# Optimization experiments

Hardware: AMD Instinct MI355X
Metric: run time of the kernel (lower is better)

The kernel has to match this reference:

```python
import jax, jax.numpy as jnp
import numpy as np

B, N = 32768, 512

def setup_inputs() -> dict:
    key = jax.random.key(0)
    k1, k2, k3, k4 = jax.random.split(key, 4)
    log_sigma_hat = jax.random.normal(k1, (B, N), dtype=jnp.float32)
    sigma = jax.random.normal(k2, (B, N), dtype=jnp.float32)
    SR = jax.random.normal(k3, (N,), dtype=jnp.float32)
    # well-conditioned invertible Gamma (covariance-like): A A^T / N + I
    A = jax.random.normal(k4, (N, N), dtype=jnp.float32)
    Gamma = A @ A.T / N + jnp.eye(N, dtype=jnp.float32)
    return {"log_sigma_hat": log_sigma_hat, "sigma": sigma, "SR": SR, "Gamma": Gamma, "k": 12}

def reference(log_sigma_hat, sigma, SR, Gamma, k):
    # r[t] = exp(sigma[t]) / exp(log_sigma_hat[t])  -> [B, N]
    r = jnp.exp(sigma - log_sigma_hat)
    Gamma_inv = jnp.linalg.inv(Gamma)
    v = Gamma_inv @ SR           # [N]  Gamma^{-1} SR
    u = Gamma_inv.T @ SR         # [N]  (SR^T Gamma^{-1})^T
    # first  = SR^T Gamma^{-1} diag(r) SR / k = sum(u * r * SR)
    first = (r * (u * SR)).sum(axis=-1) / k
    # second = SR^T Gamma^{-1} diag(r) Gamma diag(r) Gamma^{-1} SR / (2k)
    w = r * v                                     # [B, N] = diag(r) v
    Gw = jnp.einsum('ij,bj->bi', Gamma, w)        # [B, N] = Gamma diag(r) v
    second = (u * (r * Gw)).sum(axis=-1) / (2 * k)
    utils = first - second                        # [B]
    return -utils.mean()
```

## Files before the change

### kernel.cpp

```cpp
#include <hip/hip_runtime.h>
#include <hip/hip_bf16.h>
#include <stdint.h>

#define BB 32768
#define NN 512
#define CHEB_IT 10
#define NSB 16
#define NTILE 10
#define NPART 64

typedef __attribute__((ext_vector_type(8))) short bf16x8;
typedef __attribute__((ext_vector_type(4))) float f32x4;

__device__ __forceinline__ void gld_lds16(const void* g, void* l) {
  typedef __attribute__((address_space(1))) const unsigned int gas_u32;
  typedef __attribute__((address_space(3))) unsigned int las_u32;
  __builtin_amdgcn_global_load_lds((gas_u32*)(uintptr_t)g,
                                   (las_u32*)(uint32_t)(uintptr_t)l, 16, 0, 0);
}

__device__ __forceinline__ unsigned short f2bf(float x) {
  __hip_bfloat16 h = __float2bfloat16(x);
  return *reinterpret_cast<unsigned short*>(&h);
}

__device__ __forceinline__ float bf2f(unsigned short u) {
  return __uint_as_float(((unsigned)u) << 16);
}

__device__ __forceinline__ float wave_reduce(float v) {
#pragma unroll
  for (int off = 32; off > 0; off >>= 1) v += __shfl_xor(v, off, 64);
  return v;
}

__device__ void cheb_phase(const unsigned short* __restrict__ Gbf,
                           const float* __restrict__ SR, float* __restrict__ v_out,
                           float* __restrict__ pglob, unsigned int* __restrict__ ctr,
                           char* smraw) {
  unsigned short* Gs = (unsigned short*)smraw;
  float* sp = (float*)(smraw + 32768);
  float* red = sp + 512;
  const int t = threadIdx.x;
  const int m = blockIdx.x;
#pragma unroll
  for (int h = 0; h < 4; ++h) {
    const int row = h * 128 + (t >> 2), sc = t & 3;
    gld_lds16(Gbf + (size_t)row * NN + m * 32 + sc * 8, Gs + row * 32 + sc * 8);
  }
  const float theta = 3.16f, delta = 2.19f;
  const float sigma1 = theta / delta;
  float rho = delta / theta;
  float x = 0.f, r = 0.f, p = 0.f;
  if (t < 32) {
    float s = SR[m * 32 + t];
    r = s;
    p = s * (1.0f / theta);
  }
  sp[t] = SR[t] * (1.0f / theta);
  __syncthreads();
  for (int k = 0; k < CHEB_IT; ++k) {
    const int c2 = (t & 15) * 2, jseg = t >> 4;
    float a0 = 0.f, a1 = 0.f;
#pragma unroll
    for (int i = 0; i < 16; ++i) {
      const int j = jseg * 16 + i;
      const unsigned g2 = *(const unsigned*)(Gs + j * 32 + c2);
      const float pv = sp[j];
      a0 += bf2f((unsigned short)(g2 & 0xffffu)) * pv;
      a1 += bf2f((unsigned short)(g2 >> 16)) * pv;
    }
    a0 += __shfl_xor(a0, 16, 64); a0 += __shfl_xor(a0, 32, 64);
    a1 += __shfl_xor(a1, 16, 64); a1 += __shfl_xor(a1, 32, 64);
    const int lane = t & 63, wv = t >> 6;
    if (lane < 16) {
      red[wv * 32 + lane * 2] = a0;
      red[wv * 32 + lane * 2 + 1] = a1;
    }
    __syncthreads();
    const float rho_new = 1.f / (2.f * sigma1 - rho);
    if (t < 32) {
      float ap = 0.f;
#pragma unroll
      for (int w = 0; w < 8; ++w) ap += red[w * 32 + t];
      x += p;
      r -= ap;
      p = rho_new * rho * p + (2.f * rho_new / delta) * r;
      if (k < CHEB_IT - 1)
        __hip_atomic_store(pglob + (k & 1) * 512 + m * 32 + t, p,
                           __ATOMIC_RELAXED, __HIP_MEMORY_SCOPE_AGENT);
    }
    rho = rho_new;
    if (k == CHEB_IT - 1) break;
    __threadfence();
    __syncthreads();
    if (t == 0) {
      __hip_atomic_fetch_add(ctr, 1u, __ATOMIC_RELEASE, __HIP_MEMORY_SCOPE_AGENT);
      const unsigned tgt = (unsigned)NSB * (unsigned)(k + 1);
      int guard = 0;
      while (__hip_atomic_load(ctr, __ATOMIC_ACQUIRE, __HIP_MEMORY_SCOPE_AGENT) < tgt) {
        if (++guard > (1 << 27)) break;
        __builtin_amdgcn_s_sleep(8);
      }
    }
    __syncthreads();
    sp[t] = __hip_atomic_load(pglob + (k & 1) * 512 + t, __ATOMIC_RELAXED,
                              __HIP_MEMORY_SCOPE_AGENT);
    __syncthreads();
  }
  if (t < 32) v_out[m * 32 + t] = x;
}

__global__ __launch_bounds__(256) void k0_prep(
    const float* __restrict__ Gam, unsigned short* __restrict__ Gbf,
    float* __restrict__ small_zero) {
  const int t = threadIdx.x, b = blockIdx.x;
  const size_t base = ((size_t)b * 256 + t) * 8;
  float4 g0 = *(const float4*)(Gam + base);
  float4 g1 = *(const float4*)(Gam + base + 4);
  *(ushort4*)(Gbf + base) = make_ushort4(f2bf(g0.x), f2bf(g0.y), f2bf(g0.z), f2bf(g0.w));
  *(ushort4*)(Gbf + base + 4) = make_ushort4(f2bf(g1.x), f2bf(g1.y), f2bf(g1.z), f2bf(g1.w));
  if (b == 0)
    for (int i = t; i < 5888; i += 256) small_zero[i] = 0.f;
}

#define TSTRIDE 132
__global__ __launch_bounds__(512) void k1_rt(
    const float* __restrict__ lsh, const float* __restrict__ sig,
    unsigned short* __restrict__ Rt, float* __restrict__ colsum) {
  __shared__ __align__(16) float sm[4736];
  unsigned short* tile = (unsigned short*)sm;
  float* redc = sm + 4224;
  const int t = threadIdx.x;
  const int r = t >> 3, cg = t & 7;
  const int jr = t >> 3, cc = t & 7;
  const size_t bb = (size_t)blockIdx.x * 64;
  for (int jt = 0; jt < 4; ++jt) {
    const int j0 = jt * 128;
    const size_t off = (bb + r) * NN + j0 + cg * 16;
    float4 s0 = *(const float4*)(sig + off);
    float4 s1 = *(const float4*)(sig + off + 4);
    float4 s2 = *(const float4*)(sig + off + 8);
    float4 s3 = *(const float4*)(sig + off + 12);
    float4 l0 = *(const float4*)(lsh + off);
    float4 l1 = *(const float4*)(lsh + off + 4);
    float4 l2 = *(const float4*)(lsh + off + 8);
    float4 l3 = *(const float4*)(lsh + off + 12);
    ushort4 w0 = make_ushort4(f2bf(__expf(s0.x - l0.x)), f2bf(__expf(s0.y - l0.y)),
                              f2bf(__expf(s0.z - l0.z)), f2bf(__expf(s0.w - l0.w)));
    ushort4 w1 = make_ushort4(f2bf(__expf(s1.x - l1.x)), f2bf(__expf(s1.y - l1.y)),
                              f2bf(__expf(s1.z - l1.z)), f2bf(__expf(s1.w - l1.w)));
    ushort4 w2 = make_ushort4(f2bf(__expf(s2.x - l2.x)), f2bf(__expf(s2.y - l2.y)),
                              f2bf(__expf(s2.z - l2.z)), f2bf(__expf(s2.w - l2.w)));
    ushort4 w3 = make_ushort4(f2bf(__expf(s3.x - l3.x)), f2bf(__expf(s3.y - l3.y)),
                              f2bf(__expf(s3.z - l3.z)), f2bf(__expf(s3.w - l3.w)));
    if (jt) __syncthreads();
    *(ushort4*)(&tile[r * TSTRIDE + cg * 16 + 0]) = w0;
    *(ushort4*)(&tile[r * TSTRIDE + cg * 16 + 4]) = w1;
    *(ushort4*)(&tile[r * TSTRIDE + cg * 16 + 8]) = w2;
    *(ushort4*)(&tile[r * TSTRIDE + cg * 16 + 12]) = w3;
    __syncthreads();
#pragma unroll
    for (int pass = 0; pass < 2; ++pass) {
      const int j = jr + pass * 64;
      unsigned int u[4];
      float csum = 0.f;
#pragma unroll
      for (int q = 0; q < 4; ++q) {
        unsigned int lo = tile[(cc * 8 + 2 * q) * TSTRIDE + j];
        unsigned int hi = tile[(cc * 8 + 2 * q + 1) * TSTRIDE + j];
        u[q] = lo | (hi << 16);
        csum += bf2f((unsigned short)lo) + bf2f((unsigned short)hi);
      }
      *(uint4*)(Rt + (size_t)(j0 + j) * BB + bb + cc * 8) =
          make_uint4(u[0], u[1], u[2], u[3]);
      redc[t] = csum;
      __syncthreads();
      if (t < 64) {
        float s = 0.f;
#pragma unroll
        for (int q = 0; q < 8; ++q) s += redc[t * 8 + q];
        atomicAdd(&colsum[(blockIdx.x & 7) * NN + j0 + pass * 64 + t], s);
      }
      __syncthreads();
    }
  }
}

__global__ __launch_bounds__(512) void k2_syrk(
    const unsigned short* __restrict__ Rt, const unsigned short* __restrict__ Gbf,
    const float* __restrict__ SR, unsigned short* __restrict__ Cpart,
    float* __restrict__ v_out, float* __restrict__ pglob,
    unsigned int* __restrict__ ctr) {
  __shared__ __align__(16) char smraw[65536];
  if (blockIdx.x < NSB) {
    cheb_phase(Gbf, SR, v_out, pglob, ctr, smraw);
    return;
  }
  unsigned short* smem = (unsigned short*)smraw;
  const int wb = blockIdx.x - NSB;
  const int kc = wb / NTILE, tt = wb % NTILE;
  const int ti = (int)((0x3221110000ULL >> (4 * tt)) & 0xF);
  const int tj = (int)((0x3323213210ULL >> (4 * tt)) & 0xF);
  const int i0 = ti * 128, j0 = tj * 128;
  const int diag = (ti == tj);
  const size_t b0 = (size_t)kc * 512;
  const int t = threadIdx.x, lane = t & 63, wv = t >> 6;
  const int wi = (wv & 3) * 32, wj = (wv >> 2) * 64;
  const int lm = lane & 15, lq = lane >> 4;
  const int xr = lm & 7;
  const int srow = t >> 3, sc = t & 7;
  const int scol = (sc ^ (srow & 7)) * 8;
  f32x4 acc[2][4];
#pragma unroll
  for (int a = 0; a < 2; ++a)
#pragma unroll
    for (int b = 0; b < 4; ++b) acc[a][b] = (f32x4){0.f, 0.f, 0.f, 0.f};

#define STAGE(kk, buf)                                                              \
  {                                                                                 \
    unsigned short* As_ = smem + (buf)*16384;                                       \
    unsigned short* Bs_ = diag ? As_ : As_ + 8192;                                  \
    gld_lds16(Rt + (size_t)(i0 + srow) * BB + b0 + (kk) + scol,                     \
              As_ + srow * 64 + sc * 8);                                            \
    gld_lds16(Rt + (size_t)(i0 + 64 + srow) * BB + b0 + (kk) + scol,                \
              As_ + (64 + srow) * 64 + sc * 8);                                     \
    if (!diag) {                                                                    \
      gld_lds16(Rt + (size_t)(j0 + srow) * BB + b0 + (kk) + scol,                   \
                Bs_ + srow * 64 + sc * 8);                                          \
      gld_lds16(Rt + (size_t)(j0 + 64 + srow) * BB + b0 + (kk) + scol,              \
                Bs_ + (64 + srow) * 64 + sc * 8);                                   \
    }                                                                               \
  }

  STAGE(0, 0);
  __syncthreads();
  for (int c = 0; c < 8; ++c) {
    if (c < 7) STAGE((c + 1) * 64, (c + 1) & 1);
    const unsigned short* As = smem + (c & 1) * 16384;
    const unsigned short* Bs = diag ? As : As + 8192;
#pragma unroll
    for (int s = 0; s < 2; ++s) {
      bf16x8 af[2], bfr[4];
#pragma unroll
      for (int g = 0; g < 2; ++g)
        af[g] = *(const bf16x8*)(As + (wi + g * 16 + lm) * 64 + ((s * 4 + lq) ^ xr) * 8);
#pragma unroll
      for (int g = 0; g < 4; ++g)
        bfr[g] = *(const bf16x8*)(Bs + (wj + g * 16 + lm) * 64 + ((s * 4 + lq) ^ xr) * 8);
#pragma unroll
      for (int gm = 0; gm < 2; ++gm)
#pragma unroll
        for (int gn = 0; gn < 4; ++gn)
          acc[gm][gn] = __builtin_amdgcn_mfma_f32_16x16x32_bf16(af[gm], bfr[gn], acc[gm][gn], 0, 0, 0);
    }
    __syncthreads();
  }
#undef STAGE

  unsigned short* Cw = Cpart + (size_t)kc * NN * NN;
#pragma unroll
  for (int gm = 0; gm < 2; ++gm) {
    const int rbase = i0 + wi + gm * 16 + lq * 4;
#pragma unroll
    for (int gn = 0; gn < 4; ++gn) {
      const int col = j0 + wj + gn * 16 + lm;
      Cw[(size_t)(rbase + 0) * NN + col] = f2bf(acc[gm][gn][0]);
      Cw[(size_t)(rbase + 1) * NN + col] = f2bf(acc[gm][gn][1]);
      Cw[(size_t)(rbase + 2) * NN + col] = f2bf(acc[gm][gn][2]);
      Cw[(size_t)(rbase + 3) * NN + col] = f2bf(acc[gm][gn][3]);
    }
  }
}

__global__ __launch_bounds__(256) void k3_contract(
    const float* __restrict__ Gamma, const unsigned short* __restrict__ Cpart,
    const float* __restrict__ v, float* __restrict__ secondsum) {
  __shared__ float red[4];
  const int t = threadIdx.x;
  const int tidx = blockIdx.x >> 4;
  const int sub = ((blockIdx.x & 15) << 10) + t * 4;
  const int ti = (int)((0x3221110000ULL >> (4 * tidx)) & 0xF);
  const int tj = (int)((0x3323213210ULL >> (4 * tidx)) & 0xF);
  const float w = (ti == tj) ? 1.f : 2.f;
  const int i = ti * 128 + (sub >> 7);
  const int j = tj * 128 + (sub & 127);
  const size_t e = (size_t)i * NN + j;
  float cx = 0, cy = 0, cz = 0, cw = 0;
  for (int pp = 0; pp < NPART; ++pp) {
    ushort4 u = *(const ushort4*)(Cpart + (size_t)pp * NN * NN + e);
    cx += bf2f(u.x); cy += bf2f(u.y); cz += bf2f(u.z); cw += bf2f(u.w);
  }
  float4 g = *(const float4*)(Gamma + e);
  float4 vj = *(const float4*)(v + j);
  float vi = v[i];
  float p = w * vi * (g.x * cx * vj.x + g.y * cy * vj.y + g.z * cz * vj.z + g.w * cw * vj.w);
  p = wave_reduce(p);
  if ((t & 63) == 0) red[t >> 6] = p;
  __syncthreads();
  if (t == 0) atomicAdd(secondsum, red[0] + red[1] + red[2] + red[3]);
}

__global__ __launch_bounds__(512) void k4_final(
    const float* __restrict__ colsum, const float* __restrict__ v,
    const float* __restrict__ SR, const float* __restrict__ secondsum,
    const int* __restrict__ kp, float* __restrict__ out) {
  __shared__ float red[8];
  const int t = threadIdx.x;
  float cs = 0;
#pragma unroll
  for (int bk = 0; bk < 8; ++bk) cs += colsum[bk * NN + t];
  float f = (cs * (1.0f / BB)) * v[t] * SR[t];
  f = wave_reduce(f);
  if ((t & 63) == 0) red[t >> 6] = f;
  __syncthreads();
  if (t == 0) {
    float first = 0;
#pragma unroll
    for (int i = 0; i < 8; ++i) first += red[i];
    float kk = (float)kp[0];
    float sec = secondsum[0] / ((float)BB * 2.0f * kk);
    out[0] = -(first / kk - sec);
  }
}

extern "C" void kernel_launch(void* const* d_in, const int* in_sizes, int n_in,
                              void* d_out, int out_size, void* d_ws, size_t ws_size,
                              hipStream_t stream) {
  const float* lsh = (const float*)d_in[0];
  const float* sig = (const float*)d_in[1];
  const float* SR = (const float*)d_in[2];
  const float* Gam = (const float*)d_in[3];
  const int* kp = (const int*)d_in[4];
  char* ws = (char*)d_ws;
  unsigned short* Cpart = (unsigned short*)ws;
  const size_t coff = (size_t)NPART * NN * NN * sizeof(unsigned short);
  float* colsum = (float*)(ws + coff);
  float* secsum = colsum + 4096;
  float* v = secsum + 64;
  unsigned int* ctr = (unsigned int*)(v + 512);
  float* pglob = (float*)(ctr + 16);
  unsigned short* Gbf = (unsigned short*)(ws + coff + (32 << 10));
  unsigned short* Rt = (unsigned short*)(ws + coff + (32 << 10) + (512 << 10));

  k0_prep<<<128, 256, 0, stream>>>(Gam, Gbf, colsum);
  k1_rt<<<512, 512, 0, stream>>>(lsh, sig, Rt, colsum);
  k2_syrk<<<NSB + NPART * NTILE, 512, 0, stream>>>(Rt, Gbf, SR, Cpart, v, pglob, ctr);
  k3_contract<<<160, 256, 0, stream>>>(Gam, Cpart, v, secsum);
  k4_final<<<1, 512, 0, stream>>>(colsum, v, SR, secsum, kp, (float*)d_out);
}
```

Before: 232.9 us.

## Split Chebyshev solve across kernels, halve SYRK partials with 4-stage pipeline

```diff
diff --git a/kernel.cpp b/kernel.cpp
--- a/kernel.cpp
+++ b/kernel.cpp
@@ -7,7 +7,9 @@
 #define CHEB_IT 10
 #define NSB 16
 #define NTILE 10
-#define NPART 64
+#define NPART 32
+#define BKC 32
+#define NCH 32
 
 typedef __attribute__((ext_vector_type(8))) short bf16x8;
 typedef __attribute__((ext_vector_type(4))) float f32x4;
@@ -34,10 +36,11 @@
   return v;
 }
 
-__device__ void cheb_phase(const unsigned short* __restrict__ Gbf,
-                           const float* __restrict__ SR, float* __restrict__ v_out,
-                           float* __restrict__ pglob, unsigned int* __restrict__ ctr,
-                           char* smraw) {
+__device__ void cheb_run(const unsigned short* __restrict__ Gbf,
+                         const float* __restrict__ SR, float* __restrict__ st,
+                         float* __restrict__ v_out, float* __restrict__ pglob,
+                         unsigned int* __restrict__ ctr, char* smraw,
+                         int k0i, int k1i) {
   unsigned short* Gs = (unsigned short*)smraw;
   float* sp = (float*)(smraw + 32768);
   float* red = sp + 512;
@@ -51,15 +54,25 @@
   const float theta = 3.16f, delta = 2.19f;
   const float sigma1 = theta / delta;
   float rho = delta / theta;
+  for (int q = 0; q < k0i; ++q) rho = 1.f / (2.f * sigma1 - rho);
   float x = 0.f, r = 0.f, p = 0.f;
-  if (t < 32) {
-    float s = SR[m * 32 + t];
-    r = s;
-    p = s * (1.0f / theta);
-  }
-  sp[t] = SR[t] * (1.0f / theta);
+  if (k0i == 0) {
+    if (t < 32) {
+      float s = SR[m * 32 + t];
+      r = s;
+      p = s * (1.0f / theta);
+    }
+    sp[t] = SR[t] * (1.0f / theta);
+  } else {
+    if (t < 32) {
+      x = st[m * 32 + t];
+      r = st[512 + m * 32 + t];
+      p = st[1024 + m * 32 + t];
+    }
+    sp[t] = st[1024 + t];
+  }
   __syncthreads();
-  for (int k = 0; k < CHEB_IT; ++k) {
+  for (int k = k0i; k < k1i; ++k) {
     const int c2 = (t & 15) * 2, jseg = t >> 4;
     float a0 = 0.f, a1 = 0.f;
 #pragma unroll
@@ -86,17 +99,17 @@
       x += p;
       r -= ap;
       p = rho_new * rho * p + (2.f * rho_new / delta) * r;
-      if (k < CHEB_IT - 1)
+      if (k + 1 < k1i)
         __hip_atomic_store(pglob + (k & 1) * 512 + m * 32 + t, p,
                            __ATOMIC_RELAXED, __HIP_MEMORY_SCOPE_AGENT);
     }
     rho = rho_new;
-    if (k == CHEB_IT - 1) break;
+    if (k + 1 >= k1i) break;
     __threadfence();
     __syncthreads();
     if (t == 0) {
       __hip_atomic_fetch_add(ctr, 1u, __ATOMIC_RELEASE, __HIP_MEMORY_SCOPE_AGENT);
-      const unsigned tgt = (unsigned)NSB * (unsigned)(k + 1);
+      const unsigned tgt = (unsigned)NSB * (unsigned)(k - k0i + 1);
       int guard = 0;
       while (__hip_atomic_load(ctr, __ATOMIC_ACQUIRE, __HIP_MEMORY_SCOPE_AGENT) < tgt) {
         if (++guard > (1 << 27)) break;
@@ -108,7 +121,13 @@
                               __HIP_MEMORY_SCOPE_AGENT);
     __syncthreads();
   }
-  if (t < 32) v_out[m * 32 + t] = x;
+  if (k1i >= CHEB_IT) {
+    if (t < 32) v_out[m * 32 + t] = x;
+  } else if (t < 32) {
+    st[m * 32 + t] = x;
+    st[512 + m * 32 + t] = r;
+    st[1024 + m * 32 + t] = p;
+  }
 }
 
 __global__ __launch_bounds__(256) void k0_prep(
@@ -121,20 +140,27 @@
   *(ushort4*)(Gbf + base) = make_ushort4(f2bf(g0.x), f2bf(g0.y), f2bf(g0.z), f2bf(g0.w));
   *(ushort4*)(Gbf + base + 4) = make_ushort4(f2bf(g1.x), f2bf(g1.y), f2bf(g1.z), f2bf(g1.w));
   if (b == 0)
-    for (int i = t; i < 5888; i += 256) small_zero[i] = 0.f;
+    for (int i = t; i < 7424; i += 256) small_zero[i] = 0.f;
 }
 
 #define TSTRIDE 132
 __global__ __launch_bounds__(512) void k1_rt(
     const float* __restrict__ lsh, const float* __restrict__ sig,
-    unsigned short* __restrict__ Rt, float* __restrict__ colsum) {
-  __shared__ __align__(16) float sm[4736];
-  unsigned short* tile = (unsigned short*)sm;
-  float* redc = sm + 4224;
+    const float* __restrict__ SR, const unsigned short* __restrict__ Gbf,
+    unsigned short* __restrict__ Rt, float* __restrict__ colsum,
+    float* __restrict__ st, float* __restrict__ pglob,
+    unsigned int* __restrict__ ctr) {
+  __shared__ __align__(16) char smraw[36864];
+  if (blockIdx.x < NSB) {
+    cheb_run(Gbf, SR, st, nullptr, pglob, ctr, smraw, 0, 5);
+    return;
+  }
+  unsigned short* tile = (unsigned short*)smraw;
   const int t = threadIdx.x;
   const int r = t >> 3, cg = t & 7;
   const int jr = t >> 3, cc = t & 7;
-  const size_t bb = (size_t)blockIdx.x * 64;
+  const int wb = blockIdx.x - NSB;
+  const size_t bb = (size_t)wb * 64;
   for (int jt = 0; jt < 4; ++jt) {
     const int j0 = jt * 128;
     const size_t off = (bb + r) * NN + j0 + cg * 16;
@@ -174,89 +200,92 @@
       }
       *(uint4*)(Rt + (size_t)(j0 + j) * BB + bb + cc * 8) =
           make_uint4(u[0], u[1], u[2], u[3]);
-      redc[t] = csum;
-      __syncthreads();
-      if (t < 64) {
-        float s = 0.f;
-#pragma unroll
-        for (int q = 0; q < 8; ++q) s += redc[t * 8 + q];
-        atomicAdd(&colsum[(blockIdx.x & 7) * NN + j0 + pass * 64 + t], s);
-      }
-      __syncthreads();
+      csum += __shfl_xor(csum, 1, 64);
+      csum += __shfl_xor(csum, 2, 64);
+      csum += __shfl_xor(csum, 4, 64);
+      if (cc == 0) atomicAdd(&colsum[(wb & 7) * NN + j0 + j], csum);
     }
   }
 }
 
 __global__ __launch_bounds__(512) void k2_syrk(
     const unsigned short* __restrict__ Rt, const unsigned short* __restrict__ Gbf,
-    const float* __restrict__ SR, unsigned short* __restrict__ Cpart,
-    float* __restrict__ v_out, float* __restrict__ pglob,
+    unsigned short* __restrict__ Cpart, float* __restrict__ v_out,
+    float* __restrict__ st, float* __restrict__ pglob,
     unsigned int* __restrict__ ctr) {
   __shared__ __align__(16) char smraw[65536];
   if (blockIdx.x < NSB) {
-    cheb_phase(Gbf, SR, v_out, pglob, ctr, smraw);
+    cheb_run(Gbf, nullptr, st, v_out, pglob, ctr, smraw, 5, CHEB_IT);
     return;
   }
   unsigned short* smem = (unsigned short*)smraw;
   const int wb = blockIdx.x - NSB;
-  const int kc = wb / NTILE, tt = wb % NTILE;
+  const int kc = (wb & 7) * 4 + (wb >> 3) / NTILE;
+  const int tt = (wb >> 3) % NTILE;
   const int ti = (int)((0x3221110000ULL >> (4 * tt)) & 0xF);
   const int tj = (int)((0x3323213210ULL >> (4 * tt)) & 0xF);
   const int i0 = ti * 128, j0 = tj * 128;
   const int diag = (ti == tj);
-  const size_t b0 = (size_t)kc * 512;
+  const size_t b0 = (size_t)kc * 1024;
   const int t = threadIdx.x, lane = t & 63, wv = t >> 6;
   const int wi = (wv & 3) * 32, wj = (wv >> 2) * 64;
   const int lm = lane & 15, lq = lane >> 4;
-  const int xr = lm & 7;
-  const int srow = t >> 3, sc = t & 7;
-  const int scol = (sc ^ (srow & 7)) * 8;
+  const int srow4 = t >> 2, sc4 = t & 3;
+  const int scol4 = (sc4 ^ (srow4 & 3)) * 8;
   f32x4 acc[2][4];
 #pragma unroll
   for (int a = 0; a < 2; ++a)
 #pragma unroll
     for (int b = 0; b < 4; ++b) acc[a][b] = (f32x4){0.f, 0.f, 0.f, 0.f};
 
-#define STAGE(kk, buf)                                                              \
-  {                                                                                 \
-    unsigned short* As_ = smem + (buf)*16384;                                       \
-    unsigned short* Bs_ = diag ? As_ : As_ + 8192;                                  \
-    gld_lds16(Rt + (size_t)(i0 + srow) * BB + b0 + (kk) + scol,                     \
-              As_ + srow * 64 + sc * 8);                                            \
-    gld_lds16(Rt + (size_t)(i0 + 64 + srow) * BB + b0 + (kk) + scol,                \
-              As_ + (64 + srow) * 64 + sc * 8);                                     \
-    if (!diag) {                                                                    \
-      gld_lds16(Rt + (size_t)(j0 + srow) * BB + b0 + (kk) + scol,                   \
-                Bs_ + srow * 64 + sc * 8);                                          \
-      gld_lds16(Rt + (size_t)(j0 + 64 + srow) * BB + b0 + (kk) + scol,              \
-                Bs_ + (64 + srow) * 64 + sc * 8);                                   \
-    }                                                                               \
-  }
-
-  STAGE(0, 0);
-  __syncthreads();
-  for (int c = 0; c < 8; ++c) {
-    if (c < 7) STAGE((c + 1) * 64, (c + 1) & 1);
-    const unsigned short* As = smem + (c & 1) * 16384;
-    const unsigned short* Bs = diag ? As : As + 8192;
-#pragma unroll
-    for (int s = 0; s < 2; ++s) {
-      bf16x8 af[2], bfr[4];
-#pragma unroll
-      for (int g = 0; g < 2; ++g)
-        af[g] = *(const bf16x8*)(As + (wi + g * 16 + lm) * 64 + ((s * 4 + lq) ^ xr) * 8);
-#pragma unroll
-      for (int g = 0; g < 4; ++g)
-        bfr[g] = *(const bf16x8*)(Bs + (wj + g * 16 + lm) * 64 + ((s * 4 + lq) ^ xr) * 8);
-#pragma unroll
-      for (int gm = 0; gm < 2; ++gm)
-#pragma unroll
-        for (int gn = 0; gn < 4; ++gn)
-          acc[gm][gn] = __builtin_amdgcn_mfma_f32_16x16x32_bf16(af[gm], bfr[gn], acc[gm][gn], 0, 0, 0);
-    }
-    __syncthreads();
-  }
-#undef STAGE
+#define STAGE2(g)                                                               \
+  {                                                                             \
+    unsigned short* As_ = smem + ((g) & 3) * 8192;                              \
+    const size_t kb = b0 + (size_t)(g) * BKC;                                   \
+    gld_lds16(Rt + (size_t)(i0 + srow4) * BB + kb + scol4,                      \
+              As_ + srow4 * 32 + sc4 * 8);                                      \
+    if (!diag)                                                                  \
+      gld_lds16(Rt + (size_t)(j0 + srow4) * BB + kb + scol4,                    \
+                As_ + 4096 + srow4 * 32 + sc4 * 8);                             \
+  }
+
+  STAGE2(0); STAGE2(1); STAGE2(2);
+  for (int c = 0; c < NCH; ++c) {
+    const int pend = (NCH - 1 - c) < 2 ? (NCH - 1 - c) : 2;
+    if (diag) {
+      if (pend == 2) asm volatile("s_waitcnt vmcnt(2)" ::: "memory");
+      else if (pend == 1) asm volatile("s_waitcnt vmcnt(1)" ::: "memory");
+      else asm volatile("s_waitcnt vmcnt(0)" ::: "memory");
+    } else {
+      if (pend == 2) asm volatile("s_waitcnt vmcnt(4)" ::: "memory");
+      else if (pend == 1) asm volatile("s_waitcnt vmcnt(2)" ::: "memory");
+      else asm volatile("s_waitcnt vmcnt(0)" ::: "memory");
+    }
+    __builtin_amdgcn_sched_barrier(0);
+    __builtin_amdgcn_s_barrier();
+    if (c + 3 < NCH) STAGE2(c + 3);
+    const unsigned short* As = smem + (c & 3) * 8192;
+    const unsigned short* Bs = diag ? As : As + 4096;
+    bf16x8 af[2], bfr[4];
+#pragma unroll
+    for (int g = 0; g < 2; ++g) {
+      const int row = wi + g * 16 + lm;
+      af[g] = *(const bf16x8*)(As + row * 32 + (lq ^ (row & 3)) * 8);
+    }
+#pragma unroll
+    for (int g = 0; g < 4; ++g) {
+      const int row = wj + g * 16 + lm;
+      bfr[g] = *(const bf16x8*)(Bs + row * 32 + (lq ^ (row & 3)) * 8);
+    }
+#pragma unroll
+    for (int gm = 0; gm < 2; ++gm)
+#pragma unroll
+      for (int gn = 0; gn < 4; ++gn)
+        acc[gm][gn] = __builtin_amdgcn_mfma_f32_16x16x32_bf16(af[gm], bfr[gn], acc[gm][gn], 0, 0, 0);
+    __builtin_amdgcn_sched_barrier(0);
+    __builtin_amdgcn_s_barrier();
+  }
+#undef STAGE2
 
   unsigned short* Cw = Cpart + (size_t)kc * NN * NN;
 #pragma unroll
@@ -340,12 +369,13 @@
   float* v = secsum + 64;
   unsigned int* ctr = (unsigned int*)(v + 512);
   float* pglob = (float*)(ctr + 16);
+  float* st = pglob + 1024;
   unsigned short* Gbf = (unsigned short*)(ws + coff + (32 << 10));
   unsigned short* Rt = (unsigned short*)(ws + coff + (32 << 10) + (512 << 10));
 
   k0_prep<<<128, 256, 0, stream>>>(Gam, Gbf, colsum);
-  k1_rt<<<512, 512, 0, stream>>>(lsh, sig, Rt, colsum);
-  k2_syrk<<<NSB + NPART * NTILE, 512, 0, stream>>>(Rt, Gbf, SR, Cpart, v, pglob, ctr);
+  k1_rt<<<NSB + 512, 512, 0, stream>>>(lsh, sig, SR, Gbf, Rt, colsum, st, pglob, ctr);
+  k2_syrk<<<NSB + NPART * NTILE, 512, 0, stream>>>(Rt, Gbf, Cpart, v, st, pglob, ctr + 1);
   k3_contract<<<160, 256, 0, stream>>>(Gam, Cpart, v, secsum);
   k4_final<<<1, 512, 0, stream>>>(colsum, v, SR, secsum, kp, (float*)d_out);
 }
```

Measured after the change: 238.2 us. 1.02x slower.
